# Kernel optimization log

Hardware: AMD Instinct MI355X
Metric: run time of the kernel (lower is better)

## Reference

```python
import jax, jax.numpy as jnp
import numpy as np

B, OBS, NH, LAT = 8192, 256, 2048, 128

def setup_inputs() -> dict:
    key = jax.random.key(0)
    k1, k2, k3, k4, k5, k6 = jax.random.split(key, 6)
    s1 = 1.0 / np.sqrt(OBS + NH)
    s2 = 1.0 / np.sqrt(NH)
    return {
        "x": jax.random.normal(k1, (B, OBS), dtype=jnp.float32),
        "h": jax.random.normal(k2, (B, NH), dtype=jnp.float32),
        "W_i2h": jax.random.normal(k3, (NH, OBS + NH), dtype=jnp.float32) * s1,
        "b_i2h": jax.random.normal(k4, (NH,), dtype=jnp.float32) * s1,
        "W_h2o": jax.random.normal(k5, (2 * LAT, NH), dtype=jnp.float32) * s2,
        "b_h2o": jax.random.normal(k6, (2 * LAT,), dtype=jnp.float32) * s2,
    }

def reference(x, h, W_i2h, b_i2h, W_h2o, b_h2o):
    # combined = cat((x, h), dim=1)  -> [B, OBS+NH]
    combined = jnp.concatenate([x, h], axis=1)
    # h_new = tanh(i2h(combined));  Linear is y = x @ W.T + b
    h_new = jnp.tanh(combined @ W_i2h.T + b_i2h)
    out = h_new @ W_h2o.T + b_h2o  # [B, 2*LAT]
    return (out, h_new)
```

## Files before the change

### kernel.cpp

```cpp
#include <hip/hip_runtime.h>
#include <hip/hip_bf16.h>
#include <cstdint>

using bf16 = __hip_bfloat16;
typedef __attribute__((ext_vector_type(8))) short short8;
typedef __attribute__((ext_vector_type(4))) float floatx4;

static constexpr int BATCH = 8192;
static constexpr int K1    = 2304;
static constexpr int N1    = 2048;
static constexpr int K2    = 2048;
static constexpr int N2    = 256;

__device__ __forceinline__ void gload_lds16(const void* g, void* l) {
  __builtin_amdgcn_global_load_lds(
      (const __attribute__((address_space(1))) void*)g,
      (__attribute__((address_space(3))) void*)l, 16, 0, 0);
}

__device__ __forceinline__ float fast_tanh(float x) {
  float e = __builtin_amdgcn_exp2f(x * 2.8853900817779268f);
  return 1.0f - 2.0f * __builtin_amdgcn_rcpf(e + 1.0f);
}

__device__ __forceinline__ short8 cvt8(const float* src) {
  float4 a = ((const float4*)src)[0];
  float4 b = ((const float4*)src)[1];
  union { short8 v; bf16 e[8]; } u;
  u.e[0] = __float2bfloat16(a.x); u.e[1] = __float2bfloat16(a.y);
  u.e[2] = __float2bfloat16(a.z); u.e[3] = __float2bfloat16(a.w);
  u.e[4] = __float2bfloat16(b.x); u.e[5] = __float2bfloat16(b.y);
  u.e[6] = __float2bfloat16(b.z); u.e[7] = __float2bfloat16(b.w);
  return u.v;
}

static constexpr int SEG0 = BATCH * (K1 / 8);
static constexpr int SEG1 = N1 * K1 / 8;
static constexpr int SEG2 = N2 * K2 / 8;
__global__ __launch_bounds__(256) void prep(
    const float* __restrict__ x, const float* __restrict__ h,
    const float* __restrict__ W1, const float* __restrict__ W2,
    bf16* __restrict__ comb, bf16* __restrict__ W1b, bf16* __restrict__ W2b) {
  int i = blockIdx.x * 256 + threadIdx.x;
  if (i < SEG0) {
    int row  = i / 288;
    int slot = i - row * 288;
    const float* src = (slot < 32) ? (x + (size_t)row * 256 + slot * 8)
                                   : (h + (size_t)row * 2048 + (slot - 32) * 8);
    *(short8*)(comb + (size_t)row * 2304 + slot * 8) = cvt8(src);
  } else if (i < SEG0 + SEG1) {
    int j = i - SEG0;
    *(short8*)(W1b + (size_t)j * 8) = cvt8(W1 + (size_t)j * 8);
  } else {
    int j = i - (SEG0 + SEG1);
    *(short8*)(W2b + (size_t)j * 8) = cvt8(W2 + (size_t)j * 8);
  }
}

__global__ __launch_bounds__(256) void bias_init(
    const float* __restrict__ bias, float* __restrict__ out) {
  int i = blockIdx.x * 256 + threadIdx.x;
  float4 b = ((const float4*)bias)[i & 63];
  ((float4*)out)[i] = b;
}

__global__ __launch_bounds__(256) void gemm1_tanh(
    const bf16* __restrict__ A, const bf16* __restrict__ W,
    const float* __restrict__ bias,
    float* __restrict__ hf32, bf16* __restrict__ hb16) {
  __shared__ bf16 As[128 * 64];
  __shared__ bf16 Bs[128 * 64];
  const int t    = threadIdx.x;
  const int lane = t & 63;
  const int wave = t >> 6;
  const int wm   = (wave & 1) * 64;
  const int wn   = (wave >> 1) * 64;
  const int quad = lane >> 4;
  const int r15  = lane & 15;
  const int srow = t >> 3;
  const int sc   = t & 7;

  const size_t Abase = (size_t)blockIdx.x * 128 * K1;
  const size_t Bbase = (size_t)blockIdx.y * 128 * K1;

  floatx4 acc[4][4];
  const floatx4 z = {0.f, 0.f, 0.f, 0.f};
#pragma unroll
  for (int i = 0; i < 4; i++)
#pragma unroll
    for (int j = 0; j < 4; j++) acc[i][j] = z;

  for (int kt = 0; kt < K1 / 64; ++kt) {
    const int k0 = kt * 64;
    __syncthreads();
#pragma unroll
    for (int it = 0; it < 4; ++it) {
      int row = it * 32 + srow;
      int gc  = k0 + ((sc ^ (row & 7)) << 3);
      gload_lds16(A + Abase + (size_t)row * K1 + gc,
                  (char*)As + it * 4096 + t * 16);
    }
#pragma unroll
    for (int it = 0; it < 4; ++it) {
      int row = it * 32 + srow;
      int gc  = k0 + ((sc ^ (row & 7)) << 3);
      gload_lds16(W + Bbase + (size_t)row * K1 + gc,
                  (char*)Bs + it * 4096 + t * 16);
    }
    __syncthreads();
#pragma unroll
    for (int ks = 0; ks < 2; ++ks) {
      short8 af[4], bfr[4];
      const int kq = ks * 4 + quad;
#pragma unroll
      for (int mt = 0; mt < 4; ++mt) {
        int row = wm + mt * 16 + r15;
        af[mt] = *(const short8*)((const char*)As + row * 128 +
                                  ((kq ^ (row & 7)) << 4));
      }
#pragma unroll
      for (int nt = 0; nt < 4; ++nt) {
        int row = wn + nt * 16 + r15;
        bfr[nt] = *(const short8*)((const char*)Bs + row * 128 +
                                   ((kq ^ (row & 7)) << 4));
      }
#pragma unroll
      for (int mt = 0; mt < 4; ++mt)
#pragma unroll
        for (int nt = 0; nt < 4; ++nt)
          acc[mt][nt] = __builtin_amdgcn_mfma_f32_16x16x32_bf16(
              af[mt], bfr[nt], acc[mt][nt], 0, 0, 0);
    }
  }

  const int gcol0 = blockIdx.y * 128 + wn;
  float bv[4];
#pragma unroll
  for (int nt = 0; nt < 4; ++nt) bv[nt] = bias[gcol0 + nt * 16 + r15];
  const size_t grow0 = (size_t)blockIdx.x * 128 + wm;
#pragma unroll
  for (int mt = 0; mt < 4; ++mt) {
#pragma unroll
    for (int i = 0; i < 4; ++i) {
      size_t gr = grow0 + mt * 16 + quad * 4 + i;
      size_t rb = gr * (size_t)N1;
#pragma unroll
      for (int nt = 0; nt < 4; ++nt) {
        int gc = gcol0 + nt * 16 + r15;
        float v = fast_tanh(acc[mt][nt][i] + bv[nt]);
        hf32[rb + gc] = v;
        hb16[rb + gc] = __float2bfloat16(v);
      }
    }
  }
}

__global__ __launch_bounds__(256) void gemm2_out(
    const bf16* __restrict__ A, const bf16* __restrict__ W,
    float* __restrict__ out) {
  __shared__ bf16 As[32 * 64];
  __shared__ bf16 Bs[256 * 64];
  const int t    = threadIdx.x;
  const int lane = t & 63;
  const int wave = t >> 6;
  const int quad = lane >> 4;
  const int r15  = lane & 15;
  const int srow = t >> 3;
  const int sc   = t & 7;

  const int mrow0 = blockIdx.x * 32;
  const int kbase = blockIdx.y * (K2 / 2);

  floatx4 acc[2][4];
  const floatx4 z = {0.f, 0.f, 0.f, 0.f};
#pragma unroll
  for (int i = 0; i < 2; i++)
#pragma unroll
    for (int j = 0; j < 4; j++) acc[i][j] = z;

  for (int kt = 0; kt < 16; ++kt) {
    const int k0 = kbase + kt * 64;
    __syncthreads();
    {
      int row = srow;
      int gc  = k0 + ((sc ^ (row & 7)) << 3);
      gload_lds16(A + (size_t)(mrow0 + row) * K2 + gc, (char*)As + t * 16);
    }
#pragma unroll
    for (int it = 0; it < 8; ++it) {
      int row = it * 32 + srow;
      int gc  = k0 + ((sc ^ (row & 7)) << 3);
      gload_lds16(W + (size_t)row * K2 + gc,
                  (char*)Bs + it * 4096 + t * 16);
    }
    __syncthreads();
#pragma unroll
    for (int ks = 0; ks < 2; ++ks) {
      short8 af[2], bfr[4];
      const int kq = ks * 4 + quad;
#pragma unroll
      for (int mt = 0; mt < 2; ++mt) {
        int row = mt * 16 + r15;
        af[mt] = *(const short8*)((const char*)As + row * 128 +
                                  ((kq ^ (row & 7)) << 4));
      }
#pragma unroll
      for (int nt = 0; nt < 4; ++nt) {
        int row = wave * 64 + nt * 16 + r15;
        bfr[nt] = *(const short8*)((const char*)Bs + row * 128 +
                                   ((kq ^ (row & 7)) << 4));
      }
#pragma unroll
      for (int mt = 0; mt < 2; ++mt)
#pragma unroll
        for (int nt = 0; nt < 4; ++nt)
          acc[mt][nt] = __builtin_amdgcn_mfma_f32_16x16x32_bf16(
              af[mt], bfr[nt], acc[mt][nt], 0, 0, 0);
    }
  }

  const int gcol0 = wave * 64;
#pragma unroll
  for (int mt = 0; mt < 2; ++mt) {
#pragma unroll
    for (int i = 0; i < 4; ++i) {
      size_t gr = (size_t)mrow0 + mt * 16 + quad * 4 + i;
      size_t rb = gr * (size_t)N2;
#pragma unroll
      for (int nt = 0; nt < 4; ++nt) {
        int gc = gcol0 + nt * 16 + r15;
        unsafeAtomicAdd(&out[rb + gc], acc[mt][nt][i]);
      }
    }
  }
}

extern "C" void kernel_launch(void* const* d_in, const int* in_sizes, int n_in,
                              void* d_out, int out_size, void* d_ws,
                              size_t ws_size, hipStream_t stream) {
  const float* x     = (const float*)d_in[0];
  const float* h     = (const float*)d_in[1];
  const float* W_i2h = (const float*)d_in[2];
  const float* b_i2h = (const float*)d_in[3];
  const float* W_h2o = (const float*)d_in[4];
  const float* b_h2o = (const float*)d_in[5];

  float* out       = (float*)d_out;
  float* hnew_f32  = out + (size_t)BATCH * N2;

  bf16* comb   = (bf16*)d_ws;
  bf16* Wi2h_b = comb + (size_t)BATCH * K1;
  bf16* Wh2o_b = Wi2h_b + (size_t)N1 * K1;
  bf16* hnew_b = Wh2o_b + (size_t)N2 * K2;

  bias_init<<<(BATCH * N2 / 4) / 256, 256, 0, stream>>>(b_h2o, out);

  prep<<<(SEG0 + SEG1 + SEG2) / 256, 256, 0, stream>>>(
      x, h, W_i2h, W_h2o, comb, Wi2h_b, Wh2o_b);

  gemm1_tanh<<<dim3(BATCH / 128, N1 / 128), 256, 0, stream>>>(
      comb, Wi2h_b, b_i2h, hnew_f32, hnew_b);

  gemm2_out<<<dim3(BATCH / 32, 2), 256, 0, stream>>>(hnew_b, Wh2o_b, out);
}
```

Before: 278.6 us.

## Restructure gemm1 into 256x256 tiles with 8 waves and double-buffered LDS pipeline

Rewrites the first GEMM kernel so each 512-thread block computes a 256x256 tile instead of a 128x128 one. LDS is split into two buffers of half-K slices, and global-to-LDS loads for later stages are interleaved with MFMA phases using fine-grained barriers, waitcnt and s_setprio. The aim is to overlap memory loads with matrix math and raise data reuse per byte loaded. In exchange it needs 32 accumulator tiles per wave, which raises register pressure, and the hand-written synchronisation is fragile.

```diff
diff --git a/kernel.cpp b/kernel.cpp
--- a/kernel.cpp
+++ b/kernel.cpp
@@ -11,6 +11,7 @@
 static constexpr int N1    = 2048;
 static constexpr int K2    = 2048;
 static constexpr int N2    = 256;
+static constexpr int KT1   = K1 / 64;
 
 __device__ __forceinline__ void gload_lds16(const void* g, void* l) {
   __builtin_amdgcn_global_load_lds(
@@ -64,89 +65,112 @@
   ((float4*)out)[i] = b;
 }
 
-__global__ __launch_bounds__(256) void gemm1_tanh(
+__global__ __launch_bounds__(512, 2) void gemm1_tanh(
     const bf16* __restrict__ A, const bf16* __restrict__ W,
     const float* __restrict__ bias,
     float* __restrict__ hf32, bf16* __restrict__ hb16) {
-  __shared__ bf16 As[128 * 64];
-  __shared__ bf16 Bs[128 * 64];
+  __shared__ bf16 lds[2][2][2][8192];
   const int t    = threadIdx.x;
   const int lane = t & 63;
   const int wave = t >> 6;
-  const int wm   = (wave & 1) * 64;
-  const int wn   = (wave >> 1) * 64;
+  const int wm   = (wave >> 2) * 128;
+  const int wn   = (wave & 3) * 64;
   const int quad = lane >> 4;
   const int r15  = lane & 15;
-  const int srow = t >> 3;
-  const int sc   = t & 7;
-
-  const size_t Abase = (size_t)blockIdx.x * 128 * K1;
-  const size_t Bbase = (size_t)blockIdx.y * 128 * K1;
-
-  floatx4 acc[4][4];
+
+  const int srow  = t >> 2;
+  const int sslot = t & 3;
+  const int sq    = (sslot ^ (srow & 3)) * 8;
+
+  const size_t Abase = (size_t)blockIdx.x * 256 * K1;
+  const size_t Bbase = (size_t)blockIdx.y * 256 * K1;
+  const size_t gA0 = Abase + (size_t)srow * K1 + sq;
+  const size_t gA1 = Abase + (size_t)(srow + 128) * K1 + sq;
+  const size_t gB0 = Bbase + (size_t)srow * K1 + sq;
+  const size_t gB1 = Bbase + (size_t)(srow + 128) * K1 + sq;
+  const int d0 = t * 16, d1 = 8192 + t * 16;
+
+#define STAGE(sb, mat_, skh, skt) do {                                       \
+    const int ktc_ = ((skt) < KT1 ? (skt) : (KT1 - 1));                      \
+    const size_t ko_ = (size_t)ktc_ * 64 + (skh) * 32;                       \
+    const bf16* p0_ = (mat_) ? (W + gB0 + ko_) : (A + gA0 + ko_);            \
+    const bf16* p1_ = (mat_) ? (W + gB1 + ko_) : (A + gA1 + ko_);            \
+    gload_lds16(p0_, (char*)&lds[sb][mat_][skh][0] + d0);                    \
+    gload_lds16(p1_, (char*)&lds[sb][mat_][skh][0] + d1);                    \
+  } while (0)
+
+  floatx4 acc[8][4];
   const floatx4 z = {0.f, 0.f, 0.f, 0.f};
 #pragma unroll
-  for (int i = 0; i < 4; i++)
+  for (int i = 0; i < 8; i++)
 #pragma unroll
     for (int j = 0; j < 4; j++) acc[i][j] = z;
 
-  for (int kt = 0; kt < K1 / 64; ++kt) {
-    const int k0 = kt * 64;
-    __syncthreads();
-#pragma unroll
-    for (int it = 0; it < 4; ++it) {
-      int row = it * 32 + srow;
-      int gc  = k0 + ((sc ^ (row & 7)) << 3);
-      gload_lds16(A + Abase + (size_t)row * K1 + gc,
-                  (char*)As + it * 4096 + t * 16);
-    }
-#pragma unroll
-    for (int it = 0; it < 4; ++it) {
-      int row = it * 32 + srow;
-      int gc  = k0 + ((sc ^ (row & 7)) << 3);
-      gload_lds16(W + Bbase + (size_t)row * K1 + gc,
-                  (char*)Bs + it * 4096 + t * 16);
-    }
-    __syncthreads();
-#pragma unroll
-    for (int ks = 0; ks < 2; ++ks) {
-      short8 af[4], bfr[4];
-      const int kq = ks * 4 + quad;
-#pragma unroll
-      for (int mt = 0; mt < 4; ++mt) {
-        int row = wm + mt * 16 + r15;
-        af[mt] = *(const short8*)((const char*)As + row * 128 +
-                                  ((kq ^ (row & 7)) << 4));
-      }
+  STAGE(0, 0, 0, 0); STAGE(0, 1, 0, 0); STAGE(0, 0, 1, 0); STAGE(0, 1, 1, 0);
+  STAGE(1, 0, 0, 1); STAGE(1, 1, 0, 1);
+  asm volatile("s_waitcnt vmcnt(4)" ::: "memory");
+  __builtin_amdgcn_s_barrier();
+
+#define PHASE(cb, ks, mtg, sb, smat, skh, skt, VMW) do {                     \
+    short8 af_[4], bf_[4];                                                   \
+    _Pragma("unroll")                                                        \
+    for (int mt = 0; mt < 4; ++mt) {                                         \
+      const int row = wm + (mtg) * 64 + mt * 16 + r15;                       \
+      af_[mt] = *(const short8*)((const char*)&lds[cb][0][ks][0] +           \
+                                 row * 64 + ((quad ^ (row & 3)) << 4));      \
+    }                                                                        \
+    _Pragma("unroll")                                                        \
+    for (int nt = 0; nt < 4; ++nt) {                                         \
+      const int row = wn + nt * 16 + r15;                                    \
+      bf_[nt] = *(const short8*)((const char*)&lds[cb][1][ks][0] +           \
+                                 row * 64 + ((quad ^ (row & 3)) << 4));      \
+    }                                                                        \
+    STAGE(sb, smat, skh, skt);                                               \
+    __builtin_amdgcn_sched_barrier(0);                                       \
+    if (VMW) asm volatile("s_waitcnt vmcnt(4)" ::: "memory");                \
+    __builtin_amdgcn_s_barrier();                                            \
+    asm volatile("s_waitcnt lgkmcnt(0)" ::: "memory");                       \
+    __builtin_amdgcn_sched_barrier(0);                                       \
+    __builtin_amdgcn_s_setprio(1);                                           \
+    _Pragma("unroll")                                                        \
+    for (int mt = 0; mt < 4; ++mt)                                           \
+      _Pragma("unroll")                                                      \
+      for (int nt = 0; nt < 4; ++nt)                                         \
+        acc[(mtg) * 4 + mt][nt] = __builtin_amdgcn_mfma_f32_16x16x32_bf16(   \
+            af_[mt], bf_[nt], acc[(mtg) * 4 + mt][nt], 0, 0, 0);             \
+    __builtin_amdgcn_s_setprio(0);                                           \
+    __builtin_amdgcn_s_barrier();                                            \
+  } while (0)
+
+#pragma clang loop unroll(disable)
+  for (int t2 = 0; t2 < KT1 / 2; ++t2) {
+    const int n = 2 * t2;
+    PHASE(0, 0, 0,  1, 0, 1, n + 1, 0);
+    PHASE(0, 0, 1,  1, 1, 1, n + 1, 0);
+    PHASE(0, 1, 0,  0, 0, 0, n + 2, 0);
+    PHASE(0, 1, 1,  0, 1, 0, n + 2, 1);
+    PHASE(1, 0, 0,  0, 0, 1, n + 2, 0);
+    PHASE(1, 0, 1,  0, 1, 1, n + 2, 0);
+    PHASE(1, 1, 0,  1, 0, 0, n + 3, 0);
+    PHASE(1, 1, 1,  1, 1, 0, n + 3, 1);
+  }
+#undef PHASE
+#undef STAGE
+
+  const int gcol0 = blockIdx.y * 256 + wn;
+  float bv[4];
+#pragma unroll
+  for (int nt = 0; nt < 4; ++nt) bv[nt] = bias[gcol0 + nt * 16 + r15];
+  const size_t grow0 = (size_t)blockIdx.x * 256 + wm;
+#pragma unroll
+  for (int mt = 0; mt < 8; ++mt) {
+#pragma unroll
+    for (int i = 0; i < 4; ++i) {
+      const size_t gr = grow0 + mt * 16 + quad * 4 + i;
+      const size_t rb = gr * (size_t)N1;
 #pragma unroll
       for (int nt = 0; nt < 4; ++nt) {
-        int row = wn + nt * 16 + r15;
-        bfr[nt] = *(const short8*)((const char*)Bs + row * 128 +
-                                   ((kq ^ (row & 7)) << 4));
-      }
-#pragma unroll
-      for (int mt = 0; mt < 4; ++mt)
-#pragma unroll
-        for (int nt = 0; nt < 4; ++nt)
-          acc[mt][nt] = __builtin_amdgcn_mfma_f32_16x16x32_bf16(
-              af[mt], bfr[nt], acc[mt][nt], 0, 0, 0);
-    }
-  }
-
-  const int gcol0 = blockIdx.y * 128 + wn;
-  float bv[4];
-#pragma unroll
-  for (int nt = 0; nt < 4; ++nt) bv[nt] = bias[gcol0 + nt * 16 + r15];
-  const size_t grow0 = (size_t)blockIdx.x * 128 + wm;
-#pragma unroll
-  for (int mt = 0; mt < 4; ++mt) {
-#pragma unroll
-    for (int i = 0; i < 4; ++i) {
-      size_t gr = grow0 + mt * 16 + quad * 4 + i;
-      size_t rb = gr * (size_t)N1;
-#pragma unroll
-      for (int nt = 0; nt < 4; ++nt) {
-        int gc = gcol0 + nt * 16 + r15;
+        const int gc = gcol0 + nt * 16 + r15;
         float v = fast_tanh(acc[mt][nt][i] + bv[nt]);
         hf32[rb + gc] = v;
         hb16[rb + gc] = __float2bfloat16(v);
@@ -258,7 +282,7 @@
   prep<<<(SEG0 + SEG1 + SEG2) / 256, 256, 0, stream>>>(
       x, h, W_i2h, W_h2o, comb, Wi2h_b, Wh2o_b);
 
-  gemm1_tanh<<<dim3(BATCH / 128, N1 / 128), 256, 0, stream>>>(
+  gemm1_tanh<<<dim3(BATCH / 256, N1 / 256), 512, 0, stream>>>(
       comb, Wi2h_b, b_i2h, hnew_f32, hnew_b);
 
   gemm2_out<<<dim3(BATCH / 32, 2), 256, 0, stream>>>(hnew_b, Wh2o_b, out);
```

New measurement: 266.7 us. 1.04x faster.
